# Optimization experiments

Measured on AMD Instinct MI355X. Metric: run time of the kernel, lower is better.

## Reference

```python
import jax, jax.numpy as jnp
import numpy as np

T = 5
NORM_GROUPS = 8
EPS = 1e-5


def setup_inputs() -> dict:
    key = jax.random.key(0)
    inputs = jax.random.normal(key, (262144, 256), dtype=jnp.float32)
    return {"inputs": inputs}


def reference(inputs):
    g = NORM_GROUPS
    c = inputs.shape[-1] // g  # per-group channel dim (small)
    # (g, n, c): row-major flatten, exactly matching tf.reshape semantics
    Z = inputs.reshape(g, -1, c)
    Zc = Z - jnp.mean(Z, axis=1, keepdims=True)
    # per-group covariance: (g, c, c)
    S = jnp.einsum('gnc,gnd->gcd', Zc, Zc)
    S = S + EPS * jnp.eye(c, dtype=S.dtype)
    # Frobenius norm per group, keepdims -> (g, 1, 1)
    norm_S = jnp.sqrt(jnp.sum(S * S, axis=(1, 2), keepdims=True))
    S = S / norm_S
    # Newton-Schulz iteration on tiny (g, c, c) matrices
    B = jnp.broadcast_to(jnp.eye(c, dtype=S.dtype), S.shape)
    for _ in range(T):
        B = 1.5 * B - 0.5 * (B @ B @ B) @ S
    # W: (g, c, n)
    W = (B @ jnp.swapaxes(Zc, 1, 2)) / jnp.sqrt(norm_S)
    return jnp.swapaxes(W, 1, 2).reshape(inputs.shape)
```

## Files before the change

kernel.cpp:

```cpp
#include <hip/hip_runtime.h>


#define ROWS 262144
#define COLS 256
#define NG 8
#define NC 32
#define SPG 262144
#define K1_BLOCKS 1024
#define K1_BPG 128
#define K1_SAMPLES 2048
#define K1_TILES 32
#define K3_BLOCKS 2048
#define K3_BPG 256
#define K3_SAMPLES 1024
#define K3_TILES 16
#define TILE 64
#define PSTRIDE 1056
#define ZSTRIDE 40

__global__ __launch_bounds__(256) void k1_stats(const float* __restrict__ x,
                                                float* __restrict__ part) {
  __shared__ __align__(16) float zt[TILE * ZSTRIDE];
  __shared__ __align__(16) float red[4 * PSTRIDE];
  const int t = threadIdx.x;
  const int b = blockIdx.x;
  const int g = b >> 7, lb = b & 127;
  const int w = t >> 6, l = t & 63;
  const int li = l >> 3, lj = l & 7;

  float a00=0,a01=0,a02=0,a03=0;
  float a10=0,a11=0,a12=0,a13=0;
  float a20=0,a21=0,a22=0,a23=0;
  float a30=0,a31=0,a32=0,a33=0;
  float sm0=0,sm1=0,sm2=0,sm3=0;

  const float* gb = x + ((size_t)g * SPG + (size_t)lb * K1_SAMPLES) * NC;
  const int si0 = t >> 3, q0 = t & 7;
  const int si1 = (t + 256) >> 3, q1 = (t + 256) & 7;

  for (int tile = 0; tile < K1_TILES; ++tile) {
    const float* tb = gb + (size_t)tile * (TILE * NC);
    float4 v0 = *(const float4*)(tb + t * 4);
    float4 v1 = *(const float4*)(tb + (t + 256) * 4);
    __syncthreads();
    *(float4*)&zt[si0 * ZSTRIDE + q0 * 4] = v0;
    *(float4*)&zt[si1 * ZSTRIDE + q1 * 4] = v1;
    __syncthreads();
#pragma unroll
    for (int it = 0; it < 16; ++it) {
      const float* zp = &zt[(w * 16 + it) * ZSTRIDE];
      float4 zr = *(const float4*)(zp + li * 4);
      float4 zc = *(const float4*)(zp + lj * 4);
      a00 += zr.x*zc.x; a01 += zr.x*zc.y; a02 += zr.x*zc.z; a03 += zr.x*zc.w;
      a10 += zr.y*zc.x; a11 += zr.y*zc.y; a12 += zr.y*zc.z; a13 += zr.y*zc.w;
      a20 += zr.z*zc.x; a21 += zr.z*zc.y; a22 += zr.z*zc.z; a23 += zr.z*zc.w;
      a30 += zr.w*zc.x; a31 += zr.w*zc.y; a32 += zr.w*zc.z; a33 += zr.w*zc.w;
      sm0 += zr.x; sm1 += zr.y; sm2 += zr.z; sm3 += zr.w;
    }
  }
  __syncthreads();
  float* rw = &red[w * PSTRIDE];
  *(float4*)&rw[(li*4+0)*32 + lj*4] = make_float4(a00,a01,a02,a03);
  *(float4*)&rw[(li*4+1)*32 + lj*4] = make_float4(a10,a11,a12,a13);
  *(float4*)&rw[(li*4+2)*32 + lj*4] = make_float4(a20,a21,a22,a23);
  *(float4*)&rw[(li*4+3)*32 + lj*4] = make_float4(a30,a31,a32,a33);
  if (lj == 0) *(float4*)&rw[1024 + li*4] = make_float4(sm0,sm1,sm2,sm3);
  __syncthreads();
  float* po = part + (size_t)b * PSTRIDE;
  for (int e = t; e < PSTRIDE; e += 256)
    po[e] = red[e] + red[PSTRIDE+e] + red[2*PSTRIDE+e] + red[3*PSTRIDE+e];
}

__global__ __launch_bounds__(1024) void k2_solve(const float* __restrict__ part,
                                                 float* __restrict__ mt,
                                                 float* __restrict__ bias) {
  __shared__ float S[NC][NC+1], Bm[NC][NC+1], T1[NC][NC+1], T2[NC][NC+1];
  __shared__ float mu[NC];
  __shared__ float red[1024];
  const int g = blockIdx.x;
  const int t = threadIdx.x;
  const int c = t >> 5, d = t & 31;
  const float* pb = part + (size_t)g * K1_BPG * PSTRIDE;

  float gs = 0.f;
  for (int b = 0; b < K1_BPG; ++b) gs += pb[(size_t)b * PSTRIDE + t];
  if (t < NC) {
    float cs = 0.f;
    for (int b = 0; b < K1_BPG; ++b) cs += pb[(size_t)b * PSTRIDE + 1024 + t];
    mu[t] = cs * (1.f / (float)SPG);
  }
  __syncthreads();

  float Sv = gs - (float)SPG * mu[c] * mu[d] + ((c == d) ? 1e-5f : 0.f);
  red[t] = Sv * Sv;
  __syncthreads();
  for (int off = 512; off > 0; off >>= 1) {
    if (t < off) red[t] += red[t + off];
    __syncthreads();
  }
  const float normS = sqrtf(red[0]);
  S[c][d] = Sv * (1.f / normS);
  Bm[c][d] = (c == d) ? 1.f : 0.f;
  __syncthreads();

  for (int it = 0; it < 5; ++it) {
    float a = 0.f;
#pragma unroll
    for (int k = 0; k < NC; ++k) a += Bm[c][k] * Bm[k][d];
    T1[c][d] = a;
    __syncthreads();
    float b2 = 0.f;
#pragma unroll
    for (int k = 0; k < NC; ++k) b2 += T1[c][k] * Bm[k][d];
    T2[c][d] = b2;
    __syncthreads();
    float c3 = 0.f;
#pragma unroll
    for (int k = 0; k < NC; ++k) c3 += T2[c][k] * S[k][d];
    float nb = 1.5f * Bm[c][d] - 0.5f * c3;
    __syncthreads();
    Bm[c][d] = nb;
    __syncthreads();
  }

  const float Mv = Bm[c][d] * (1.f / sqrtf(normS));
  mt[g * 1024 + d * 32 + c] = Mv;
  red[t] = Mv * mu[d];
  __syncthreads();
  for (int off = 16; off > 0; off >>= 1) {
    if (d < off) red[t] += red[t + off];
    __syncthreads();
  }
  if (d == 0) bias[g * 32 + c] = red[t];
}

__global__ __launch_bounds__(256) void k3_apply(const float* __restrict__ x,
                                                const float* __restrict__ mt,
                                                const float* __restrict__ bias,
                                                float* __restrict__ out) {
  __shared__ __align__(16) float Mt[1024];
  __shared__ __align__(16) float zt[TILE * ZSTRIDE];
  const int t = threadIdx.x;
  const int b = blockIdx.x;
  const int g = b >> 8, lb = b & 255;
  const int k = t & 7, sl = t >> 3;

  *(float4*)&Mt[t * 4] = *(const float4*)&mt[g * 1024 + t * 4];
  float4 bi = *(const float4*)&bias[g * 32 + k * 4];
  const size_t base = ((size_t)g * SPG + (size_t)lb * K3_SAMPLES) * NC;
  const int si0 = t >> 3, q0 = t & 7;
  const int si1 = (t + 256) >> 3, q1 = (t + 256) & 7;

  for (int tile = 0; tile < K3_TILES; ++tile) {
    const float* tb = x + base + (size_t)tile * (TILE * NC);
    float4 v0 = *(const float4*)(tb + t * 4);
    float4 v1 = *(const float4*)(tb + (t + 256) * 4);
    __syncthreads();
    *(float4*)&zt[si0 * ZSTRIDE + q0 * 4] = v0;
    *(float4*)&zt[si1 * ZSTRIDE + q1 * 4] = v1;
    __syncthreads();

    float acc0[4] = {0,0,0,0}, acc1[4] = {0,0,0,0};
    const float* z0 = &zt[sl * ZSTRIDE];
    const float* z1 = &zt[(sl + 32) * ZSTRIDE];
#pragma unroll
    for (int dq = 0; dq < 8; ++dq) {
      float4 za4 = *(const float4*)(z0 + dq * 4);
      float4 zb4 = *(const float4*)(z1 + dq * 4);
      const float* za = (const float*)&za4;
      const float* zb = (const float*)&zb4;
#pragma unroll
      for (int dd = 0; dd < 4; ++dd) {
        float4 m4 = *(const float4*)&Mt[(dq * 4 + dd) * 32 + k * 4];
        acc0[0] += m4.x * za[dd]; acc0[1] += m4.y * za[dd];
        acc0[2] += m4.z * za[dd]; acc0[3] += m4.w * za[dd];
        acc1[0] += m4.x * zb[dd]; acc1[1] += m4.y * zb[dd];
        acc1[2] += m4.z * zb[dd]; acc1[3] += m4.w * zb[dd];
      }
    }
    float* ob = out + base + (size_t)tile * (TILE * NC);
    *(float4*)(ob + sl * 32 + k * 4) =
        make_float4(acc0[0]-bi.x, acc0[1]-bi.y, acc0[2]-bi.z, acc0[3]-bi.w);
    *(float4*)(ob + (sl + 32) * 32 + k * 4) =
        make_float4(acc1[0]-bi.x, acc1[1]-bi.y, acc1[2]-bi.z, acc1[3]-bi.w);
  }
}

extern "C" void kernel_launch(void* const* d_in, const int* in_sizes, int n_in,
                              void* d_out, int out_size, void* d_ws, size_t ws_size,
                              hipStream_t stream) {
  (void)in_sizes; (void)n_in; (void)out_size; (void)ws_size;
  const float* x = (const float*)d_in[0];
  float* out = (float*)d_out;
  float* ws = (float*)d_ws;
  float* part = ws;
  float* mt   = ws + (size_t)K1_BLOCKS * PSTRIDE;
  float* bias = mt + NG * 1024;

  k1_stats<<<K1_BLOCKS, 256, 0, stream>>>(x, part);
  k2_solve<<<NG, 1024, 0, stream>>>(part, mt, bias);
  k3_apply<<<K3_BLOCKS, 256, 0, stream>>>(x, mt, bias, out);
}
```

Before: 531.3 us.

## Enlarge register tiles in stats, solve and apply kernels to raise reuse

The covariance kernel now gives each thread an 8x8 accumulator tile over 4 sample subsets and reduces them across lanes with shuffles. The Newton-Schulz solve uses 256 threads, each computing a float4 row segment from padded shared matrices. The apply kernel processes 128-row tiles with 4 row groups per thread. The aim is fewer shared-memory loads per FMA and fewer barriers, at the cost of higher register pressure and possible occupancy loss.

```diff
diff --git a/kernel.cpp b/kernel.cpp
--- a/kernel.cpp
+++ b/kernel.cpp
@@ -13,68 +13,94 @@
 #define K3_BLOCKS 2048
 #define K3_BPG 256
 #define K3_SAMPLES 1024
-#define K3_TILES 16
+#define K3_TILES 8
 #define TILE 64
+#define K3_TILE 128
 #define PSTRIDE 1056
-#define ZSTRIDE 40
+#define ZS1 36
+#define ZS3 40
 
 __global__ __launch_bounds__(256) void k1_stats(const float* __restrict__ x,
                                                 float* __restrict__ part) {
-  __shared__ __align__(16) float zt[TILE * ZSTRIDE];
+  __shared__ __align__(16) float zt[TILE * ZS1];
   __shared__ __align__(16) float red[4 * PSTRIDE];
   const int t = threadIdx.x;
   const int b = blockIdx.x;
   const int g = b >> 7, lb = b & 127;
-  const int w = t >> 6, l = t & 63;
-  const int li = l >> 3, lj = l & 7;
-
-  float a00=0,a01=0,a02=0,a03=0;
-  float a10=0,a11=0,a12=0,a13=0;
-  float a20=0,a21=0,a22=0,a23=0;
-  float a30=0,a31=0,a32=0,a33=0;
-  float sm0=0,sm1=0,sm2=0,sm3=0;
+  const int w = t >> 6;
+  const int l = t & 63;
+  const int q = l >> 4;
+  const int p = l & 15;
+  const int li = p >> 2, lj = p & 3;
+
+  float acc[8][8] = {{0.f}};
+  float sm[8] = {0.f};
 
   const float* gb = x + ((size_t)g * SPG + (size_t)lb * K1_SAMPLES) * NC;
   const int si0 = t >> 3, q0 = t & 7;
-  const int si1 = (t + 256) >> 3, q1 = (t + 256) & 7;
+  const int si1 = (t + 256) >> 3;
 
   for (int tile = 0; tile < K1_TILES; ++tile) {
     const float* tb = gb + (size_t)tile * (TILE * NC);
     float4 v0 = *(const float4*)(tb + t * 4);
     float4 v1 = *(const float4*)(tb + (t + 256) * 4);
     __syncthreads();
-    *(float4*)&zt[si0 * ZSTRIDE + q0 * 4] = v0;
-    *(float4*)&zt[si1 * ZSTRIDE + q1 * 4] = v1;
-    __syncthreads();
-#pragma unroll
-    for (int it = 0; it < 16; ++it) {
-      const float* zp = &zt[(w * 16 + it) * ZSTRIDE];
-      float4 zr = *(const float4*)(zp + li * 4);
-      float4 zc = *(const float4*)(zp + lj * 4);
-      a00 += zr.x*zc.x; a01 += zr.x*zc.y; a02 += zr.x*zc.z; a03 += zr.x*zc.w;
-      a10 += zr.y*zc.x; a11 += zr.y*zc.y; a12 += zr.y*zc.z; a13 += zr.y*zc.w;
-      a20 += zr.z*zc.x; a21 += zr.z*zc.y; a22 += zr.z*zc.z; a23 += zr.z*zc.w;
-      a30 += zr.w*zc.x; a31 += zr.w*zc.y; a32 += zr.w*zc.z; a33 += zr.w*zc.w;
-      sm0 += zr.x; sm1 += zr.y; sm2 += zr.z; sm3 += zr.w;
-    }
-  }
-  __syncthreads();
-  float* rw = &red[w * PSTRIDE];
-  *(float4*)&rw[(li*4+0)*32 + lj*4] = make_float4(a00,a01,a02,a03);
-  *(float4*)&rw[(li*4+1)*32 + lj*4] = make_float4(a10,a11,a12,a13);
-  *(float4*)&rw[(li*4+2)*32 + lj*4] = make_float4(a20,a21,a22,a23);
-  *(float4*)&rw[(li*4+3)*32 + lj*4] = make_float4(a30,a31,a32,a33);
-  if (lj == 0) *(float4*)&rw[1024 + li*4] = make_float4(sm0,sm1,sm2,sm3);
+    *(float4*)&zt[si0 * ZS1 + q0 * 4] = v0;
+    *(float4*)&zt[si1 * ZS1 + q0 * 4] = v1;
+    __syncthreads();
+#pragma unroll
+    for (int it = 0; it < 4; ++it) {
+      const float* zp = &zt[(w * 16 + it * 4 + q) * ZS1];
+      float4 r0 = *(const float4*)(zp + li * 8);
+      float4 r1 = *(const float4*)(zp + li * 8 + 4);
+      float4 c0 = *(const float4*)(zp + lj * 8);
+      float4 c1 = *(const float4*)(zp + lj * 8 + 4);
+      float rr[8] = {r0.x, r0.y, r0.z, r0.w, r1.x, r1.y, r1.z, r1.w};
+      float cc[8] = {c0.x, c0.y, c0.z, c0.w, c1.x, c1.y, c1.z, c1.w};
+#pragma unroll
+      for (int i = 0; i < 8; ++i) {
+        sm[i] += rr[i];
+#pragma unroll
+        for (int j = 0; j < 8; ++j) acc[i][j] += rr[i] * cc[j];
+      }
+    }
+  }
+
+#pragma unroll
+  for (int i = 0; i < 8; ++i) {
+#pragma unroll
+    for (int j = 0; j < 8; ++j) {
+      acc[i][j] += __shfl_xor(acc[i][j], 16);
+      acc[i][j] += __shfl_xor(acc[i][j], 32);
+    }
+    sm[i] += __shfl_xor(sm[i], 16);
+    sm[i] += __shfl_xor(sm[i], 32);
+  }
+
+  if (q == 0) {
+    float* rw = &red[w * PSTRIDE];
+#pragma unroll
+    for (int i = 0; i < 8; ++i) {
+      *(float4*)&rw[(li * 8 + i) * 32 + lj * 8] =
+          make_float4(acc[i][0], acc[i][1], acc[i][2], acc[i][3]);
+      *(float4*)&rw[(li * 8 + i) * 32 + lj * 8 + 4] =
+          make_float4(acc[i][4], acc[i][5], acc[i][6], acc[i][7]);
+    }
+    if (lj == 0) {
+      *(float4*)&rw[1024 + li * 8] = make_float4(sm[0], sm[1], sm[2], sm[3]);
+      *(float4*)&rw[1024 + li * 8 + 4] = make_float4(sm[4], sm[5], sm[6], sm[7]);
+    }
+  }
   __syncthreads();
   float* po = part + (size_t)b * PSTRIDE;
   for (int e = t; e < PSTRIDE; e += 256)
-    po[e] = red[e] + red[PSTRIDE+e] + red[2*PSTRIDE+e] + red[3*PSTRIDE+e];
+    po[e] = red[e] + red[PSTRIDE + e] + red[2 * PSTRIDE + e] + red[3 * PSTRIDE + e];
 }
 
 __global__ __launch_bounds__(1024) void k2_solve(const float* __restrict__ part,
                                                  float* __restrict__ mt,
                                                  float* __restrict__ bias) {
-  __shared__ float S[NC][NC+1], Bm[NC][NC+1], T1[NC][NC+1], T2[NC][NC+1];
+  __shared__ __align__(16) float S[NC * 36], Bm[NC * 36], T1[NC * 36], T2[NC * 36];
   __shared__ float mu[NC];
   __shared__ float red[1024];
   const int g = blockIdx.x;
@@ -99,31 +125,53 @@
     __syncthreads();
   }
   const float normS = sqrtf(red[0]);
-  S[c][d] = Sv * (1.f / normS);
-  Bm[c][d] = (c == d) ? 1.f : 0.f;
-  __syncthreads();
-
+  S[c * 36 + d] = Sv * (1.f / normS);
+  Bm[c * 36 + d] = (c == d) ? 1.f : 0.f;
+  __syncthreads();
+
+  const int c2 = t >> 3, d4 = (t & 7) * 4;
   for (int it = 0; it < 5; ++it) {
-    float a = 0.f;
-#pragma unroll
-    for (int k = 0; k < NC; ++k) a += Bm[c][k] * Bm[k][d];
-    T1[c][d] = a;
-    __syncthreads();
-    float b2 = 0.f;
-#pragma unroll
-    for (int k = 0; k < NC; ++k) b2 += T1[c][k] * Bm[k][d];
-    T2[c][d] = b2;
-    __syncthreads();
-    float c3 = 0.f;
-#pragma unroll
-    for (int k = 0; k < NC; ++k) c3 += T2[c][k] * S[k][d];
-    float nb = 1.5f * Bm[c][d] - 0.5f * c3;
-    __syncthreads();
-    Bm[c][d] = nb;
-    __syncthreads();
-  }
-
-  const float Mv = Bm[c][d] * (1.f / sqrtf(normS));
+    if (t < 256) {
+      float4 a = make_float4(0.f, 0.f, 0.f, 0.f);
+#pragma unroll
+      for (int kk = 0; kk < NC; ++kk) {
+        const float s = Bm[c2 * 36 + kk];
+        const float4 b4 = *(const float4*)&Bm[kk * 36 + d4];
+        a.x += s * b4.x; a.y += s * b4.y; a.z += s * b4.z; a.w += s * b4.w;
+      }
+      *(float4*)&T1[c2 * 36 + d4] = a;
+    }
+    __syncthreads();
+    if (t < 256) {
+      float4 a = make_float4(0.f, 0.f, 0.f, 0.f);
+#pragma unroll
+      for (int kk = 0; kk < NC; ++kk) {
+        const float s = T1[c2 * 36 + kk];
+        const float4 b4 = *(const float4*)&Bm[kk * 36 + d4];
+        a.x += s * b4.x; a.y += s * b4.y; a.z += s * b4.z; a.w += s * b4.w;
+      }
+      *(float4*)&T2[c2 * 36 + d4] = a;
+    }
+    __syncthreads();
+    if (t < 256) {
+      float4 a = make_float4(0.f, 0.f, 0.f, 0.f);
+#pragma unroll
+      for (int kk = 0; kk < NC; ++kk) {
+        const float s = T2[c2 * 36 + kk];
+        const float4 b4 = *(const float4*)&S[kk * 36 + d4];
+        a.x += s * b4.x; a.y += s * b4.y; a.z += s * b4.z; a.w += s * b4.w;
+      }
+      float4 bm = *(const float4*)&Bm[c2 * 36 + d4];
+      bm.x = 1.5f * bm.x - 0.5f * a.x;
+      bm.y = 1.5f * bm.y - 0.5f * a.y;
+      bm.z = 1.5f * bm.z - 0.5f * a.z;
+      bm.w = 1.5f * bm.w - 0.5f * a.w;
+      *(float4*)&Bm[c2 * 36 + d4] = bm;
+    }
+    __syncthreads();
+  }
+
+  const float Mv = Bm[c * 36 + d] * (1.f / sqrtf(normS));
   mt[g * 1024 + d * 32 + c] = Mv;
   red[t] = Mv * mu[d];
   __syncthreads();
@@ -139,7 +187,7 @@
                                                 const float* __restrict__ bias,
                                                 float* __restrict__ out) {
   __shared__ __align__(16) float Mt[1024];
-  __shared__ __align__(16) float zt[TILE * ZSTRIDE];
+  __shared__ __align__(16) float zt[K3_TILE * ZS3];
   const int t = threadIdx.x;
   const int b = blockIdx.x;
   const int g = b >> 8, lb = b & 255;
@@ -148,27 +196,36 @@
   *(float4*)&Mt[t * 4] = *(const float4*)&mt[g * 1024 + t * 4];
   float4 bi = *(const float4*)&bias[g * 32 + k * 4];
   const size_t base = ((size_t)g * SPG + (size_t)lb * K3_SAMPLES) * NC;
-  const int si0 = t >> 3, q0 = t & 7;
-  const int si1 = (t + 256) >> 3, q1 = (t + 256) & 7;
 
   for (int tile = 0; tile < K3_TILES; ++tile) {
-    const float* tb = x + base + (size_t)tile * (TILE * NC);
+    const float* tb = x + base + (size_t)tile * (K3_TILE * NC);
     float4 v0 = *(const float4*)(tb + t * 4);
-    float4 v1 = *(const float4*)(tb + (t + 256) * 4);
-    __syncthreads();
-    *(float4*)&zt[si0 * ZSTRIDE + q0 * 4] = v0;
-    *(float4*)&zt[si1 * ZSTRIDE + q1 * 4] = v1;
-    __syncthreads();
-
-    float acc0[4] = {0,0,0,0}, acc1[4] = {0,0,0,0};
-    const float* z0 = &zt[sl * ZSTRIDE];
-    const float* z1 = &zt[(sl + 32) * ZSTRIDE];
+    float4 v1 = *(const float4*)(tb + t * 4 + 1024);
+    float4 v2 = *(const float4*)(tb + t * 4 + 2048);
+    float4 v3 = *(const float4*)(tb + t * 4 + 3072);
+    __syncthreads();
+    *(float4*)&zt[sl * ZS3 + k * 4] = v0;
+    *(float4*)&zt[(sl + 32) * ZS3 + k * 4] = v1;
+    *(float4*)&zt[(sl + 64) * ZS3 + k * 4] = v2;
+    *(float4*)&zt[(sl + 96) * ZS3 + k * 4] = v3;
+    __syncthreads();
+
+    float acc0[4] = {0, 0, 0, 0}, acc1[4] = {0, 0, 0, 0};
+    float acc2[4] = {0, 0, 0, 0}, acc3[4] = {0, 0, 0, 0};
+    const float* z0 = &zt[sl * ZS3];
+    const float* z1 = &zt[(sl + 32) * ZS3];
+    const float* z2 = &zt[(sl + 64) * ZS3];
+    const float* z3 = &zt[(sl + 96) * ZS3];
 #pragma unroll
     for (int dq = 0; dq < 8; ++dq) {
       float4 za4 = *(const float4*)(z0 + dq * 4);
       float4 zb4 = *(const float4*)(z1 + dq * 4);
+      float4 zc4 = *(const float4*)(z2 + dq * 4);
+      float4 zd4 = *(const float4*)(z3 + dq * 4);
       const float* za = (const float*)&za4;
       const float* zb = (const float*)&zb4;
+      const float* zc = (const float*)&zc4;
+      const float* zd = (const float*)&zd4;
 #pragma unroll
       for (int dd = 0; dd < 4; ++dd) {
         float4 m4 = *(const float4*)&Mt[(dq * 4 + dd) * 32 + k * 4];
@@ -176,13 +233,21 @@
         acc0[2] += m4.z * za[dd]; acc0[3] += m4.w * za[dd];
         acc1[0] += m4.x * zb[dd]; acc1[1] += m4.y * zb[dd];
         acc1[2] += m4.z * zb[dd]; acc1[3] += m4.w * zb[dd];
-      }
-    }
-    float* ob = out + base + (size_t)tile * (TILE * NC);
+        acc2[0] += m4.x * zc[dd]; acc2[1] += m4.y * zc[dd];
+        acc2[2] += m4.z * zc[dd]; acc2[3] += m4.w * zc[dd];
+        acc3[0] += m4.x * zd[dd]; acc3[1] += m4.y * zd[dd];
+        acc3[2] += m4.z * zd[dd]; acc3[3] += m4.w * zd[dd];
+      }
+    }
+    float* ob = out + base + (size_t)tile * (K3_TILE * NC);
     *(float4*)(ob + sl * 32 + k * 4) =
-        make_float4(acc0[0]-bi.x, acc0[1]-bi.y, acc0[2]-bi.z, acc0[3]-bi.w);
+        make_float4(acc0[0] - bi.x, acc0[1] - bi.y, acc0[2] - bi.z, acc0[3] - bi.w);
     *(float4*)(ob + (sl + 32) * 32 + k * 4) =
-        make_float4(acc1[0]-bi.x, acc1[1]-bi.y, acc1[2]-bi.z, acc1[3]-bi.w);
+        make_float4(acc1[0] - bi.x, acc1[1] - bi.y, acc1[2] - bi.z, acc1[3] - bi.w);
+    *(float4*)(ob + (sl + 64) * 32 + k * 4) =
+        make_float4(acc2[0] - bi.x, acc2[1] - bi.y, acc2[2] - bi.z, acc2[3] - bi.w);
+    *(float4*)(ob + (sl + 96) * 32 + k * 4) =
+        make_float4(acc3[0] - bi.x, acc3[1] - bi.y, acc3[2] - bi.z, acc3[3] - bi.w);
   }
 }
 
```

Result: no change. 533.9 us (+0.5%).
